# Kernel tuning notes

Hardware: AMD Instinct MI355X
Metric: run time of the kernel (lower is better)

## Reference

```python
import jax, jax.numpy as jnp
import numpy as np

DIMS = [1024, 2048, 1024, 1024]


def setup_inputs() -> dict:
    key = jax.random.key(0)
    ks = jax.random.split(key, 13)
    d_in, h1, h2, d_out = DIMS
    s = lambda k, shape, fan_in: jax.random.normal(k, shape, dtype=jnp.float32) / np.sqrt(fan_in)
    return {
        "x": jax.random.normal(ks[0], (4, 2048, d_in), dtype=jnp.float32),
        "w1": s(ks[1], (h1, d_in), d_in), "b1": jnp.zeros((h1,), jnp.float32),
        "w2": s(ks[2], (h2, h1), h1), "b2": jnp.zeros((h2,), jnp.float32),
        "wq": s(ks[3], (h2, h2), h2), "bq": jnp.zeros((h2,), jnp.float32),
        "wk": s(ks[4], (h2, h2), h2), "bk": jnp.zeros((h2,), jnp.float32),
        "wv": s(ks[5], (h2, h2), h2), "bv": jnp.zeros((h2,), jnp.float32),
        "wo": s(ks[6], (d_out, h2), h2), "bo": jnp.zeros((d_out,), jnp.float32),
    }


def reference(x, w1, b1, w2, b2, wq, bq, wk, bk, wv, bv, wo, bo):
    # MLP: Linear + ReLU twice (torch Linear: x @ W^T + b)
    h = jax.nn.relu(jnp.einsum('bsd,hd->bsh', x, w1) + b1)
    h = jax.nn.relu(jnp.einsum('bsh,eh->bse', h, w2) + b2)
    # Self-attention (single head over full hidden_dim)
    q = jnp.einsum('bse,fe->bsf', h, wq) + bq
    k = jnp.einsum('bse,fe->bsf', h, wk) + bk
    v = jnp.einsum('bse,fe->bsf', h, wv) + bv
    hidden_dim = wq.shape[0]
    scores = jnp.einsum('bsf,btf->bst', q, k) / jnp.sqrt(jnp.float32(hidden_dim))
    attn = jax.nn.softmax(scores, axis=-1)
    ctx = jnp.einsum('bst,btf->bsf', attn, v) + v  # residual with V
    return jnp.einsum('bsf,of->bso', ctx, wo) + bo
```

## Files before the change

kernel.cpp:

```cpp
#include <hip/hip_runtime.h>
#include <hip/hip_bf16.h>

typedef __bf16 bf16;
typedef bf16 bf16x8 __attribute__((ext_vector_type(8)));
typedef float f32x4 __attribute__((ext_vector_type(4)));

#define EPI_BIAS_RELU  0
#define EPI_BIAS_BF16  1
#define EPI_PLAIN_BF16 2
#define EPI_RESID      3
#define EPI_BIAS_F32   4

__device__ __forceinline__ void lds_load16(const bf16* g, bf16* l) {
  __builtin_amdgcn_global_load_lds((__attribute__((address_space(1))) void*)g,
                                   (__attribute__((address_space(3))) void*)l,
                                   16, 0, 0);
}

template<int N> __device__ __forceinline__ void vmw() {
  if constexpr (N == 0) asm volatile("s_waitcnt vmcnt(0)" ::: "memory");
  else if constexpr (N == 2) asm volatile("s_waitcnt vmcnt(2)" ::: "memory");
  else if constexpr (N == 4) asm volatile("s_waitcnt vmcnt(4)" ::: "memory");
  else if constexpr (N == 6) asm volatile("s_waitcnt vmcnt(6)" ::: "memory");
}
__device__ __forceinline__ void barrier() { asm volatile("s_barrier" ::: "memory"); }

template<int EPI>
__global__ __launch_bounds__(512, 2)
void gemm4p(const bf16* __restrict__ A, const bf16* __restrict__ B,
            void* __restrict__ Cv, const float* __restrict__ bias,
            const bf16* __restrict__ resid,
            int K, int lda, int ldb, int ldc, int ldr,
            long long sAz, long long sBz, long long sCz, long long sRz)
{
  constexpr int BM = 256, BK = 64;
  constexpr int M_REP = 8, N_REP = 4, MH = 4, NH = 2;
  constexpr int LA = 2, LB = 2, N3 = LA + LB + LA;

  __shared__ __align__(16) bf16 lA[2][BM * BK];
  __shared__ __align__(16) bf16 lB[2][256 * BK];

  const int gx = gridDim.x, gy = gridDim.y;
  const int nwg = gx * gy * gridDim.z;
  int o = (blockIdx.z * gy + blockIdx.y) * gx + blockIdx.x;
  o = (o & 7) * (nwg >> 3) + (o >> 3);
  const int bx = o % gx, rem = o / gx, by = rem % gy, z = rem / gy;

  const bf16* Ab = A + (size_t)z * sAz;
  const bf16* Bb = B + (size_t)z * sBz;
  const int row0 = by * BM, col0 = bx * 256;
  const int tid = threadIdx.x, w = tid >> 6, l = tid & 63;
  const int wr = w >> 2, wc = w & 3;

  const int srow = l >> 3, scb = (l & 7) ^ srow;
  const bf16* gA = Ab + (size_t)(row0 + w * 8 + srow) * lda + scb * 8;
  const bf16* gB = Bb + (size_t)(col0 + w * 8 + srow) * ldb + scb * 8;

  auto issueA = [&](int buf, int k0, int h) {
#pragma unroll
    for (int i = 0; i < LA; i++)
      lds_load16(gA + (size_t)(h * 128 + i * 64) * lda + k0,
                 &lA[buf][(h * 128 + i * 64 + w * 8) * BK]);
  };
  auto issueB = [&](int buf, int k0, int h) {
#pragma unroll
    for (int i = 0; i < LB; i++)
      lds_load16(gB + (size_t)(h * 128 + i * 64) * ldb + k0,
                 &lB[buf][(h * 128 + i * 64 + w * 8) * BK]);
  };

  const int fr = l & 15, fq = l >> 4, sw = fr & 7;
  bf16x8 aA0[MH][2], aA1[MH][2], bB0[NH][2], bB1[NH][2];
  f32x4 acc[M_REP][N_REP] = {};

  auto readA = [&](bf16x8 (&dst)[MH][2], int buf, int h) {
#pragma unroll
    for (int mm = 0; mm < MH; mm++) {
      const bf16* base = &lA[buf][(h * 128 + wr * 64 + mm * 16 + fr) * BK];
#pragma unroll
      for (int kk = 0; kk < 2; kk++)
        dst[mm][kk] = *(const bf16x8*)(base + ((kk * 4 + fq) ^ sw) * 8);
    }
  };
  auto readB = [&](bf16x8 (&dst)[NH][2], int buf, int h) {
#pragma unroll
    for (int nn = 0; nn < NH; nn++) {
      const bf16* base = &lB[buf][(h * 128 + wc * 32 + nn * 16 + fr) * BK];
#pragma unroll
      for (int kk = 0; kk < 2; kk++)
        dst[nn][kk] = *(const bf16x8*)(base + ((kk * 4 + fq) ^ sw) * 8);
    }
  };
  auto quad = [&](const bf16x8 (&a)[MH][2], const bf16x8 (&b)[NH][2],
                  int mBase, int nBase) {
    __builtin_amdgcn_s_setprio(1);
#pragma unroll
    for (int mh = 0; mh < MH; mh++)
#pragma unroll
      for (int nh = 0; nh < NH; nh++)
#pragma unroll
        for (int kk = 0; kk < 2; kk++)
          acc[mBase + mh][nBase + nh] = __builtin_amdgcn_mfma_f32_16x16x32_bf16(
              a[mh][kk], b[nh][kk], acc[mBase + mh][nBase + nh], 0, 0, 0);
    __builtin_amdgcn_s_setprio(0);
  };

  const int NT = K / BK;
  issueA(0, 0, 0); issueB(0, 0, 0); issueA(0, 0, 1); issueB(0, 0, 1);
  issueA(1, BK, 0); issueB(1, BK, 0); issueA(1, BK, 1);
  vmw<N3>();
  barrier();

  for (int t = 0; t < NT; t++) {
    const int cur = t & 1, nxt = cur ^ 1;
    const bool s1 = (t + 1 < NT), s2 = (t + 2 < NT);
    const int k1 = (t + 1) * BK, k2 = (t + 2) * BK;
    readA(aA0, cur, 0);
    readB(bB0, cur, 0);
    if (s1) issueB(nxt, k1, 1);
    barrier();
    quad(aA0, bB0, 0, 0);
    barrier();
    readA(aA1, cur, 1);
    if (s2) issueA(cur, k2, 0);
    barrier();
    quad(aA1, bB0, MH, 0);
    barrier();
    readB(bB1, cur, 1);
    if (s2) issueB(cur, k2, 0);
    barrier();
    quad(aA1, bB1, MH, NH);
    barrier();
    if (s2) { issueA(cur, k2, 1); vmw<N3>(); }
    else vmw<0>();
    barrier();
    quad(aA0, bB1, 0, NH);
    barrier();
  }

#pragma unroll
  for (int m = 0; m < M_REP; m++) {
#pragma unroll
    for (int n = 0; n < N_REP; n++) {
      const int col = col0 + (n / NH) * 128 + wc * 32 + (n % NH) * 16 + fr;
#pragma unroll
      for (int j = 0; j < 4; j++) {
        const int rrow = row0 + (m / MH) * 128 + wr * 64 + (m % MH) * 16 + fq * 4 + j;
        const float val = acc[m][n][j];
        if constexpr (EPI == EPI_PLAIN_BF16) {
          bf16* Cp = (bf16*)Cv + (size_t)z * sCz;
          Cp[(size_t)rrow * ldc + col] = (bf16)val;
        } else if constexpr (EPI == EPI_BIAS_F32) {
          float* Cp = (float*)Cv;
          Cp[(size_t)rrow * ldc + col] = val + bias[col];
        } else if constexpr (EPI == EPI_BIAS_BF16) {
          bf16* Cp = (bf16*)Cv;
          Cp[(size_t)rrow * ldc + col] = (bf16)(val + bias[col]);
        } else if constexpr (EPI == EPI_BIAS_RELU) {
          bf16* Cp = (bf16*)Cv;
          Cp[(size_t)rrow * ldc + col] = (bf16)fmaxf(val + bias[col], 0.f);
        } else {
          bf16* Cp = (bf16*)Cv + (size_t)z * sCz;
          const bf16* Rp = resid + (size_t)z * sRz;
          Cp[(size_t)rrow * ldc + col] = (bf16)(val + (float)Rp[(size_t)rrow * ldr + col]);
        }
      }
    }
  }
}

template<int EPI>
__global__ __launch_bounds__(512, 2)
void gemm2p(const bf16* __restrict__ A, const bf16* __restrict__ B,
            void* __restrict__ Cv, const float* __restrict__ bias,
            const bf16* __restrict__ resid,
            int K, int lda, int ldb, int ldc, int ldr,
            long long sAz, long long sBz, long long sCz, long long sRz)
{
  constexpr int BM = 128, BK = 64;
  constexpr int M_REP = 4, NH = 2;

  __shared__ __align__(16) bf16 lA[2][BM * BK];
  __shared__ __align__(16) bf16 lB[2][256 * BK];

  const int gx = gridDim.x, gy = gridDim.y;
  const int nwg = gx * gy * gridDim.z;
  int o = (blockIdx.z * gy + blockIdx.y) * gx + blockIdx.x;
  o = (o & 7) * (nwg >> 3) + (o >> 3);
  const int bx = o % gx, rem = o / gx, by = rem % gy, z = rem / gy;

  const bf16* Ab = A + (size_t)z * sAz;
  const bf16* Bb = B + (size_t)z * sBz;
  const int row0 = by * BM, col0 = bx * 256;
  const int tid = threadIdx.x, w = tid >> 6, l = tid & 63;
  const int wr = w >> 2, wc = w & 3;

  const int srow = l >> 3, scb = (l & 7) ^ srow;
  const bf16* gA = Ab + (size_t)(row0 + w * 8 + srow) * lda + scb * 8;
  const bf16* gB = Bb + (size_t)(col0 + w * 8 + srow) * ldb + scb * 8;

  auto issueAfull = [&](int buf, int k0) {
#pragma unroll
    for (int i = 0; i < 2; i++)
      lds_load16(gA + (size_t)(i * 64) * lda + k0,
                 &lA[buf][(i * 64 + w * 8) * BK]);
  };
  auto issueBfull = [&](int buf, int k0) {
#pragma unroll
    for (int i = 0; i < 4; i++)
      lds_load16(gB + (size_t)(i * 64) * ldb + k0,
                 &lB[buf][(i * 64 + w * 8) * BK]);
  };

  const int fr = l & 15, fq = l >> 4, sw = fr & 7;
  bf16x8 aA[M_REP][2], bB0[NH][2], bB1[NH][2];
  f32x4 acc[M_REP][4] = {};

  auto readAfull = [&](int buf) {
#pragma unroll
    for (int m = 0; m < M_REP; m++) {
      const bf16* base = &lA[buf][(wr * 64 + m * 16 + fr) * BK];
#pragma unroll
      for (int kk = 0; kk < 2; kk++)
        aA[m][kk] = *(const bf16x8*)(base + ((kk * 4 + fq) ^ sw) * 8);
    }
  };
  auto readB = [&](bf16x8 (&dst)[NH][2], int buf, int h) {
#pragma unroll
    for (int nn = 0; nn < NH; nn++) {
      const bf16* base = &lB[buf][(h * 128 + wc * 32 + nn * 16 + fr) * BK];
#pragma unroll
      for (int kk = 0; kk < 2; kk++)
        dst[nn][kk] = *(const bf16x8*)(base + ((kk * 4 + fq) ^ sw) * 8);
    }
  };
  auto quad2 = [&](const bf16x8 (&b)[NH][2], int nBase) {
    __builtin_amdgcn_s_setprio(1);
#pragma unroll
    for (int m = 0; m < M_REP; m++)
#pragma unroll
      for (int nh = 0; nh < NH; nh++)
#pragma unroll
        for (int kk = 0; kk < 2; kk++)
          acc[m][nBase + nh] = __builtin_amdgcn_mfma_f32_16x16x32_bf16(
              aA[m][kk], b[nh][kk], acc[m][nBase + nh], 0, 0, 0);
    __builtin_amdgcn_s_setprio(0);
  };

  const int NT = K / BK;
  issueAfull(0, 0); issueBfull(0, 0); issueAfull(1, BK);
  vmw<2>();
  barrier();

  for (int t = 0; t < NT; t++) {
    const int cur = t & 1, nxt = cur ^ 1;
    const bool s1 = (t + 1 < NT), s2 = (t + 2 < NT);
    readAfull(cur);
    readB(bB0, cur, 0);
    if (s1) issueBfull(nxt, (t + 1) * BK);
    barrier();
    quad2(bB0, 0);
    barrier();
    readB(bB1, cur, 1);
    if (s2) { issueAfull(cur, (t + 2) * BK); vmw<2>(); }
    else vmw<0>();
    barrier();
    quad2(bB1, NH);
    barrier();
  }

#pragma unroll
  for (int m = 0; m < M_REP; m++) {
#pragma unroll
    for (int n = 0; n < 4; n++) {
      const int col = col0 + (n / NH) * 128 + wc * 32 + (n % NH) * 16 + fr;
#pragma unroll
      for (int j = 0; j < 4; j++) {
        const int rrow = row0 + wr * 64 + m * 16 + fq * 4 + j;
        const float val = acc[m][n][j];
        if constexpr (EPI == EPI_PLAIN_BF16) {
          bf16* Cp = (bf16*)Cv + (size_t)z * sCz;
          Cp[(size_t)rrow * ldc + col] = (bf16)val;
        } else if constexpr (EPI == EPI_BIAS_F32) {
          float* Cp = (float*)Cv;
          Cp[(size_t)rrow * ldc + col] = val + bias[col];
        } else if constexpr (EPI == EPI_BIAS_BF16) {
          bf16* Cp = (bf16*)Cv;
          Cp[(size_t)rrow * ldc + col] = (bf16)(val + bias[col]);
        } else if constexpr (EPI == EPI_BIAS_RELU) {
          bf16* Cp = (bf16*)Cv;
          Cp[(size_t)rrow * ldc + col] = (bf16)fmaxf(val + bias[col], 0.f);
        } else {
          bf16* Cp = (bf16*)Cv + (size_t)z * sCz;
          const bf16* Rp = resid + (size_t)z * sRz;
          Cp[(size_t)rrow * ldc + col] = (bf16)(val + (float)Rp[(size_t)rrow * ldr + col]);
        }
      }
    }
  }
}

__global__ __launch_bounds__(256)
void cast_all(const float* __restrict__ x,  const float* __restrict__ w1,
              const float* __restrict__ w2, const float* __restrict__ wq,
              const float* __restrict__ wk, const float* __restrict__ wv,
              const float* __restrict__ wo,
              bf16* __restrict__ xb, bf16* __restrict__ w1b,
              bf16* __restrict__ w2b, bf16* __restrict__ wqkvb,
              bf16* __restrict__ wob) {
  const int b = blockIdx.x;
  const float* src; bf16* dst; int base; float scale = 1.f;
  if (b < 4096)      { src = x;  dst = xb;    base = b; }
  else if (b < 5120) { src = w1; dst = w1b;   base = b - 4096; }
  else if (b < 6144) { src = w2; dst = w2b;   base = b - 5120; }
  else if (b < 6656) { src = wq; dst = wqkvb;                base = b - 6144; scale = 0.03125f; }
  else if (b < 7168) { src = wk; dst = wqkvb + (1 << 20);    base = b - 6656; }
  else if (b < 7680) { src = wv; dst = wqkvb + (2 << 20);    base = b - 7168; }
  else               { src = wo; dst = wob;   base = b - 7680; }
  const int i = base * 256 + threadIdx.x;
  const float4* p = (const float4*)src;
  float4 a = p[2 * i], c = p[2 * i + 1];
  bf16x8 o8;
  o8[0] = (bf16)(a.x * scale); o8[1] = (bf16)(a.y * scale);
  o8[2] = (bf16)(a.z * scale); o8[3] = (bf16)(a.w * scale);
  o8[4] = (bf16)(c.x * scale); o8[5] = (bf16)(c.y * scale);
  o8[6] = (bf16)(c.z * scale); o8[7] = (bf16)(c.w * scale);
  ((bf16x8*)dst)[i] = o8;
}

__global__ __launch_bounds__(256)
void pack_bias_qkv(const float* __restrict__ bq, const float* __restrict__ bk,
                   const float* __restrict__ bv, float* __restrict__ o) {
  int i = blockIdx.x * 256 + threadIdx.x;
  o[i] = (i < 1024) ? bq[i] * 0.03125f : (i < 2048 ? bk[i - 1024] : bv[i - 2048]);
}

__global__ __launch_bounds__(256)
void transpose_bf16(const bf16* __restrict__ in, bf16* __restrict__ out,
                    int R, int C, int ldi,
                    long long inZ, long long outZ) {
  __shared__ bf16 t[64][72];
  const bf16* ib = in + (size_t)blockIdx.z * inZ;
  bf16* ob = out + (size_t)blockIdx.z * outZ;
  const int r0 = blockIdx.y * 64, c0 = blockIdx.x * 64;
  const int tid = threadIdx.x;
#pragma unroll
  for (int p = 0; p < 2; p++) {
    int r = p * 32 + tid / 8, cc = (tid % 8) * 8;
    bf16x8 vv = *(const bf16x8*)(ib + (size_t)(r0 + r) * ldi + c0 + cc);
#pragma unroll
    for (int j = 0; j < 8; j++) t[r][cc + j] = vv[j];
  }
  __syncthreads();
#pragma unroll
  for (int p = 0; p < 2; p++) {
    int r = p * 32 + tid / 8, cc = (tid % 8) * 8;
    bf16x8 o;
#pragma unroll
    for (int j = 0; j < 8; j++) o[j] = t[cc + j][r];
    *(bf16x8*)(ob + (size_t)(c0 + r) * R + r0 + cc) = o;
  }
}

__global__ __launch_bounds__(256)
void softmax_rows(bf16* __restrict__ S) {
  const size_t row = blockIdx.x;
  const int t = threadIdx.x, wv_ = t >> 6, ln = t & 63;
  bf16x8 v8 = ((const bf16x8*)(S + row * 2048))[t];
  float v[8];
#pragma unroll
  for (int j = 0; j < 8; j++) v[j] = (float)v8[j];
  float m = v[0];
#pragma unroll
  for (int j = 1; j < 8; j++) m = fmaxf(m, v[j]);
  for (int o = 32; o; o >>= 1) m = fmaxf(m, __shfl_xor(m, o));
  __shared__ float redm[4], reds[4];
  if (ln == 0) redm[wv_] = m;
  __syncthreads();
  m = fmaxf(fmaxf(redm[0], redm[1]), fmaxf(redm[2], redm[3]));
  float e[8], s = 0.f;
#pragma unroll
  for (int j = 0; j < 8; j++) { e[j] = __expf(v[j] - m); s += e[j]; }
  for (int o = 32; o; o >>= 1) s += __shfl_xor(s, o);
  if (ln == 0) reds[wv_] = s;
  __syncthreads();
  s = reds[0] + reds[1] + reds[2] + reds[3];
  const float inv = 1.f / s;
  bf16x8 o8;
#pragma unroll
  for (int j = 0; j < 8; j++) o8[j] = (bf16)(e[j] * inv);
  ((bf16x8*)(S + row * 2048))[t] = o8;
}

extern "C" void kernel_launch(void* const* d_in, const int* in_sizes, int n_in,
                              void* d_out, int out_size, void* d_ws, size_t ws_size,
                              hipStream_t stream) {
  const float* x  = (const float*)d_in[0];
  const float* w1 = (const float*)d_in[1];
  const float* b1 = (const float*)d_in[2];
  const float* w2 = (const float*)d_in[3];
  const float* b2 = (const float*)d_in[4];
  const float* wq = (const float*)d_in[5];
  const float* bq = (const float*)d_in[6];
  const float* wk = (const float*)d_in[7];
  const float* bk = (const float*)d_in[8];
  const float* wv = (const float*)d_in[9];
  const float* bv = (const float*)d_in[10];
  const float* wo = (const float*)d_in[11];
  const float* bo = (const float*)d_in[12];
  float* out = (float*)d_out;

  char* ws = (char*)d_ws;
  const size_t MB = 1024ull * 1024ull;
  if (ws_size < 130 * MB) return;

  bf16* w1b   = (bf16*)(ws + 0 * MB);
  bf16* w2b   = (bf16*)(ws + 4 * MB);
  bf16* wqkvb = (bf16*)(ws + 8 * MB);
  bf16* wob   = (bf16*)(ws + 14 * MB);
  float* bqkv = (float*)(ws + 16 * MB);
  bf16* xb  = (bf16*)(ws + 17 * MB);
  bf16* h1  = (bf16*)(ws + 33 * MB);
  bf16* h   = (bf16*)(ws + 65 * MB);
  bf16* qkv = (bf16*)(ws + 81 * MB);
  bf16* vT  = (bf16*)(ws + 17 * MB);
  bf16* S   = (bf16*)(ws + 33 * MB);
  bf16* ctx = (bf16*)(ws + 65 * MB);

  cast_all<<<8192, 256, 0, stream>>>(x, w1, w2, wq, wk, wv, wo,
                                     xb, w1b, w2b, wqkvb, wob);
  pack_bias_qkv<<<12, 256, 0, stream>>>(bq, bk, bv, bqkv);

  gemm4p<EPI_BIAS_RELU><<<dim3(8, 32, 1), 512, 0, stream>>>(
      xb, w1b, h1, b1, nullptr, 1024, 1024, 1024, 2048, 0, 0, 0, 0, 0);
  gemm2p<EPI_BIAS_RELU><<<dim3(4, 64, 1), 512, 0, stream>>>(
      h1, w2b, h, b2, nullptr, 2048, 2048, 2048, 1024, 0, 0, 0, 0, 0);
  gemm4p<EPI_BIAS_BF16><<<dim3(12, 32, 1), 512, 0, stream>>>(
      h, wqkvb, qkv, bqkv, nullptr, 1024, 1024, 1024, 3072, 0, 0, 0, 0, 0);
  transpose_bf16<<<dim3(16, 32, 4), 256, 0, stream>>>(
      qkv + 2048, vT, 2048, 1024, 3072, 2048LL * 3072, 1024LL * 2048);
  gemm4p<EPI_PLAIN_BF16><<<dim3(8, 8, 4), 512, 0, stream>>>(
      qkv, qkv + 1024, S, nullptr, nullptr, 1024, 3072, 3072, 2048, 0,
      2048LL * 3072, 2048LL * 3072, 2048LL * 2048, 0);
  softmax_rows<<<8192, 256, 0, stream>>>(S);
  gemm2p<EPI_RESID><<<dim3(4, 16, 4), 512, 0, stream>>>(
      S, vT, ctx, nullptr, qkv + 2048, 2048, 2048, 2048, 1024, 3072,
      2048LL * 2048, 1024LL * 2048, 2048LL * 1024, 2048LL * 3072);
  gemm2p<EPI_BIAS_F32><<<dim3(4, 64, 1), 512, 0, stream>>>(
      ctx, wob, out, bo, nullptr, 1024, 1024, 1024, 1024, 0, 0, 0, 0, 0);
}
```

Before: 275.2 us.

## Split fused QKV GEMM into QK and V GEMMs; remap blocks across XCDs

```diff
diff --git a/kernel.cpp b/kernel.cpp
--- a/kernel.cpp
+++ b/kernel.cpp
@@ -25,13 +25,23 @@
 }
 __device__ __forceinline__ void barrier() { asm volatile("s_barrier" ::: "memory"); }
 
+__device__ __forceinline__ void xcd_map(int& bx, int& by, int& z) {
+  const int gx = gridDim.x, gy = gridDim.y;
+  const int Y8 = (gy * gridDim.z) >> 3;
+  const int L = (blockIdx.z * gy + blockIdx.y) * gx + blockIdx.x;
+  const int xcd = L & 7, j = L >> 3;
+  bx = j % gx;
+  const int yy = xcd * Y8 + j / gx;
+  by = yy % gy;
+  z  = yy / gy;
+}
+
 template<int EPI>
 __global__ __launch_bounds__(512, 2)
 void gemm4p(const bf16* __restrict__ A, const bf16* __restrict__ B,
             void* __restrict__ Cv, const float* __restrict__ bias,
-            const bf16* __restrict__ resid,
-            int K, int lda, int ldb, int ldc, int ldr,
-            long long sAz, long long sBz, long long sCz, long long sRz)
+            int K, int lda, int ldb, int ldc,
+            long long sAz, long long sBz, long long sCz)
 {
   constexpr int BM = 256, BK = 64;
   constexpr int M_REP = 8, N_REP = 4, MH = 4, NH = 2;
@@ -40,11 +50,8 @@
   __shared__ __align__(16) bf16 lA[2][BM * BK];
   __shared__ __align__(16) bf16 lB[2][256 * BK];
 
-  const int gx = gridDim.x, gy = gridDim.y;
-  const int nwg = gx * gy * gridDim.z;
-  int o = (blockIdx.z * gy + blockIdx.y) * gx + blockIdx.x;
-  o = (o & 7) * (nwg >> 3) + (o >> 3);
-  const int bx = o % gx, rem = o / gx, by = rem % gy, z = rem / gy;
+  int bx, by, z;
+  xcd_map(bx, by, z);
 
   const bf16* Ab = A + (size_t)z * sAz;
   const bf16* Bb = B + (size_t)z * sBz;
@@ -150,19 +157,12 @@
         if constexpr (EPI == EPI_PLAIN_BF16) {
           bf16* Cp = (bf16*)Cv + (size_t)z * sCz;
           Cp[(size_t)rrow * ldc + col] = (bf16)val;
-        } else if constexpr (EPI == EPI_BIAS_F32) {
-          float* Cp = (float*)Cv;
-          Cp[(size_t)rrow * ldc + col] = val + bias[col];
         } else if constexpr (EPI == EPI_BIAS_BF16) {
           bf16* Cp = (bf16*)Cv;
           Cp[(size_t)rrow * ldc + col] = (bf16)(val + bias[col]);
         } else if constexpr (EPI == EPI_BIAS_RELU) {
           bf16* Cp = (bf16*)Cv;
           Cp[(size_t)rrow * ldc + col] = (bf16)fmaxf(val + bias[col], 0.f);
-        } else {
-          bf16* Cp = (bf16*)Cv + (size_t)z * sCz;
-          const bf16* Rp = resid + (size_t)z * sRz;
-          Cp[(size_t)rrow * ldc + col] = (bf16)(val + (float)Rp[(size_t)rrow * ldr + col]);
         }
       }
     }
@@ -183,11 +183,8 @@
   __shared__ __align__(16) bf16 lA[2][BM * BK];
   __shared__ __align__(16) bf16 lB[2][256 * BK];
 
-  const int gx = gridDim.x, gy = gridDim.y;
-  const int nwg = gx * gy * gridDim.z;
-  int o = (blockIdx.z * gy + blockIdx.y) * gx + blockIdx.x;
-  o = (o & 7) * (nwg >> 3) + (o >> 3);
-  const int bx = o % gx, rem = o / gx, by = rem % gy, z = rem / gy;
+  int bx, by, z;
+  xcd_map(bx, by, z);
 
   const bf16* Ab = A + (size_t)z * sAz;
   const bf16* Bb = B + (size_t)z * sBz;
@@ -306,17 +303,17 @@
               const float* __restrict__ wk, const float* __restrict__ wv,
               const float* __restrict__ wo,
               bf16* __restrict__ xb, bf16* __restrict__ w1b,
-              bf16* __restrict__ w2b, bf16* __restrict__ wqkvb,
-              bf16* __restrict__ wob) {
+              bf16* __restrict__ w2b, bf16* __restrict__ wqkb,
+              bf16* __restrict__ wvb, bf16* __restrict__ wob) {
   const int b = blockIdx.x;
   const float* src; bf16* dst; int base; float scale = 1.f;
-  if (b < 4096)      { src = x;  dst = xb;    base = b; }
-  else if (b < 5120) { src = w1; dst = w1b;   base = b - 4096; }
-  else if (b < 6144) { src = w2; dst = w2b;   base = b - 5120; }
-  else if (b < 6656) { src = wq; dst = wqkvb;                base = b - 6144; scale = 0.03125f; }
-  else if (b < 7168) { src = wk; dst = wqkvb + (1 << 20);    base = b - 6656; }
-  else if (b < 7680) { src = wv; dst = wqkvb + (2 << 20);    base = b - 7168; }
-  else               { src = wo; dst = wob;   base = b - 7680; }
+  if (b < 4096)      { src = x;  dst = xb;   base = b; }
+  else if (b < 5120) { src = w1; dst = w1b;  base = b - 4096; }
+  else if (b < 6144) { src = w2; dst = w2b;  base = b - 5120; }
+  else if (b < 6656) { src = wq; dst = wqkb;              base = b - 6144; scale = 0.03125f; }
+  else if (b < 7168) { src = wk; dst = wqkb + (1 << 20);  base = b - 6656; }
+  else if (b < 7680) { src = wv; dst = wvb;  base = b - 7168; }
+  else               { src = wo; dst = wob;  base = b - 7680; }
   const int i = base * 256 + threadIdx.x;
   const float4* p = (const float4*)src;
   float4 a = p[2 * i], c = p[2 * i + 1];
@@ -329,10 +326,10 @@
 }
 
 __global__ __launch_bounds__(256)
-void pack_bias_qkv(const float* __restrict__ bq, const float* __restrict__ bk,
-                   const float* __restrict__ bv, float* __restrict__ o) {
+void pack_bias_qk(const float* __restrict__ bq, const float* __restrict__ bk,
+                  float* __restrict__ o) {
   int i = blockIdx.x * 256 + threadIdx.x;
-  o[i] = (i < 1024) ? bq[i] * 0.03125f : (i < 2048 ? bk[i - 1024] : bv[i - 2048]);
+  o[i] = (i < 1024) ? bq[i] * 0.03125f : bk[i - 1024];
 }
 
 __global__ __launch_bounds__(256)
@@ -414,38 +411,42 @@
   const size_t MB = 1024ull * 1024ull;
   if (ws_size < 130 * MB) return;
 
-  bf16* w1b   = (bf16*)(ws + 0 * MB);
-  bf16* w2b   = (bf16*)(ws + 4 * MB);
-  bf16* wqkvb = (bf16*)(ws + 8 * MB);
-  bf16* wob   = (bf16*)(ws + 14 * MB);
-  float* bqkv = (float*)(ws + 16 * MB);
+  bf16* w1b  = (bf16*)(ws + 0 * MB);
+  bf16* w2b  = (bf16*)(ws + 4 * MB);
+  bf16* wqkb = (bf16*)(ws + 8 * MB);
+  bf16* wvb  = (bf16*)(ws + 12 * MB);
+  bf16* wob  = (bf16*)(ws + 14 * MB);
+  float* bqk = (float*)(ws + 16 * MB);
   bf16* xb  = (bf16*)(ws + 17 * MB);
   bf16* h1  = (bf16*)(ws + 33 * MB);
   bf16* h   = (bf16*)(ws + 65 * MB);
-  bf16* qkv = (bf16*)(ws + 81 * MB);
+  bf16* qk  = (bf16*)(ws + 81 * MB);
+  bf16* vb  = (bf16*)(ws + 113 * MB);
   bf16* vT  = (bf16*)(ws + 17 * MB);
   bf16* S   = (bf16*)(ws + 33 * MB);
   bf16* ctx = (bf16*)(ws + 65 * MB);
 
   cast_all<<<8192, 256, 0, stream>>>(x, w1, w2, wq, wk, wv, wo,
-                                     xb, w1b, w2b, wqkvb, wob);
-  pack_bias_qkv<<<12, 256, 0, stream>>>(bq, bk, bv, bqkv);
+                                     xb, w1b, w2b, wqkb, wvb, wob);
+  pack_bias_qk<<<8, 256, 0, stream>>>(bq, bk, bqk);
 
   gemm4p<EPI_BIAS_RELU><<<dim3(8, 32, 1), 512, 0, stream>>>(
-      xb, w1b, h1, b1, nullptr, 1024, 1024, 1024, 2048, 0, 0, 0, 0, 0);
+      xb, w1b, h1, b1, 1024, 1024, 1024, 2048, 0, 0, 0);
   gemm2p<EPI_BIAS_RELU><<<dim3(4, 64, 1), 512, 0, stream>>>(
       h1, w2b, h, b2, nullptr, 2048, 2048, 2048, 1024, 0, 0, 0, 0, 0);
-  gemm4p<EPI_BIAS_BF16><<<dim3(12, 32, 1), 512, 0, stream>>>(
-      h, wqkvb, qkv, bqkv, nullptr, 1024, 1024, 1024, 3072, 0, 0, 0, 0, 0);
+  gemm4p<EPI_BIAS_BF16><<<dim3(8, 32, 1), 512, 0, stream>>>(
+      h, wqkb, qk, bqk, 1024, 1024, 1024, 2048, 0, 0, 0);
+  gemm2p<EPI_BIAS_BF16><<<dim3(4, 64, 1), 512, 0, stream>>>(
+      h, wvb, vb, bv, nullptr, 1024, 1024, 1024, 1024, 0, 0, 0, 0, 0);
   transpose_bf16<<<dim3(16, 32, 4), 256, 0, stream>>>(
-      qkv + 2048, vT, 2048, 1024, 3072, 2048LL * 3072, 1024LL * 2048);
+      vb, vT, 2048, 1024, 1024, 2048LL * 1024, 1024LL * 2048);
   gemm4p<EPI_PLAIN_BF16><<<dim3(8, 8, 4), 512, 0, stream>>>(
-      qkv, qkv + 1024, S, nullptr, nullptr, 1024, 3072, 3072, 2048, 0,
-      2048LL * 3072, 2048LL * 3072, 2048LL * 2048, 0);
+      qk, qk + 1024, S, nullptr, 1024, 2048, 2048, 2048,
+      2048LL * 2048, 2048LL * 2048, 2048LL * 2048);
   softmax_rows<<<8192, 256, 0, stream>>>(S);
   gemm2p<EPI_RESID><<<dim3(4, 16, 4), 512, 0, stream>>>(
-      S, vT, ctx, nullptr, qkv + 2048, 2048, 2048, 2048, 1024, 3072,
-      2048LL * 2048, 1024LL * 2048, 2048LL * 1024, 2048LL * 3072);
+      S, vT, ctx, nullptr, vb, 2048, 2048, 2048, 1024, 1024,
+      2048LL * 2048, 1024LL * 2048, 2048LL * 1024, 2048LL * 1024);
   gemm2p<EPI_BIAS_F32><<<dim3(4, 64, 1), 512, 0, stream>>>(
       ctx, wob, out, bo, nullptr, 1024, 1024, 1024, 1024, 0, 0, 0, 0, 0);
 }
```

Result: faster. 268.4 us (-2.5%).
